# Kernel optimization log

Measured on AMD Instinct MI355X. Metric: run time of the kernel, lower is better.

Reference implementation:

```python
import jax, jax.numpy as jnp
import numpy as np

DIM, HEAD, FFN = 256, 4, 1024
NEG = -1e9


def layer_norm(x, g, b, eps=1e-5):
    mu = jnp.mean(x, axis=-1, keepdims=True)
    var = jnp.mean((x - mu) ** 2, axis=-1, keepdims=True)
    return (x - mu) / jnp.sqrt(var + eps) * g + b


def setup_inputs() -> dict:
    key = jax.random.key(0)
    ks = jax.random.split(key, 10)
    B, T, D = 8, 2048, DIM
    s = 1.0 / np.sqrt(D)
    x = jax.random.normal(ks[0], (B, T, D), dtype=jnp.float32)
    mask = jax.random.randint(ks[1], (B, T), 0, 2).astype(jnp.float32)
    Wqkv = jax.random.uniform(ks[2], (3 * D, D), jnp.float32, -s, s)
    bqkv = jnp.zeros((3 * D,), jnp.float32)
    Wo = jax.random.uniform(ks[3], (D, D), jnp.float32, -s, s)
    bo = jnp.zeros((D,), jnp.float32)
    W1 = jax.random.uniform(ks[4], (FFN, D), jnp.float32, -s, s)
    b1 = jnp.zeros((FFN,), jnp.float32)
    W2 = jax.random.uniform(ks[5], (D, FFN), jnp.float32, -1.0 / np.sqrt(FFN), 1.0 / np.sqrt(FFN))
    b2 = jnp.zeros((D,), jnp.float32)
    g1 = jnp.ones((D,), jnp.float32); be1 = jnp.zeros((D,), jnp.float32)
    g2 = jnp.ones((D,), jnp.float32); be2 = jnp.zeros((D,), jnp.float32)
    return dict(x=x, mask=mask, Wqkv=Wqkv, bqkv=bqkv, Wo=Wo, bo=bo,
                W1=W1, b1=b1, W2=W2, b2=b2, g1=g1, be1=be1, g2=g2, be2=be2)


def _forward(x, mask, Wqkv, bqkv, Wo, bo, W1, b1, W2, b2, g1, be1, g2, be2):
    B, T, D = x.shape
    H = HEAD
    hd = D // H
    # --- MultiheadAttention (explicit, non-flash path, need_weights=True) ---
    qkv = jnp.einsum('btd,ed->bte', x, Wqkv) + bqkv            # (B,T,3D)
    q, k, v = jnp.split(qkv, 3, axis=-1)
    q = q.reshape(B, T, H, hd).transpose(0, 2, 1, 3)           # (B,H,T,hd)
    k = k.reshape(B, T, H, hd).transpose(0, 2, 1, 3)
    v = v.reshape(B, T, H, hd).transpose(0, 2, 1, 3)
    scores = jnp.einsum('bhqd,bhkd->bhqk', q, k) / jnp.sqrt(jnp.float32(hd))
    scores = jnp.where(mask[:, None, None, :] > 0.5, NEG, scores)
    w = jax.nn.softmax(scores, axis=-1)                        # (B,H,T,T)
    attn = jnp.einsum('bhqk,bhkd->bhqd', w, v)                 # (B,H,T,hd)
    attn = attn.transpose(0, 2, 1, 3).reshape(B, T, D)
    attn_out = jnp.einsum('btd,ed->bte', attn, Wo) + bo        # (B,T,D)
    w_avg = jnp.mean(w, axis=1)                                # (B,T,T), averaged over heads
    # halting score: sum over query dim (dim=1), then masked softmax
    halting = jnp.sum(w_avg, axis=1)                           # (B,T)
    halting = jax.nn.softmax(halting + mask * (-1e10), axis=-1)
    # --- residual + LN + FFN + LN ---
    h = layer_norm(x + attn_out, g1, be1)
    ffn = jnp.einsum('btf,df->btd', jax.nn.relu(jnp.einsum('btd,fd->btf', h, W1) + b1), W2) + b2
    out = layer_norm(h + ffn, g2, be2)
    return out, halting


def reference(x, mask, Wqkv, bqkv, Wo, bo, W1, b1, W2, b2, g1, be1, g2, be2):
    return _forward(x, mask, Wqkv, bqkv, Wo, bo, W1, b1, W2, b2, g1, be1, g2, be2)
```

## Files before the change

kernel.cpp:

```cpp
#include <hip/hip_runtime.h>
#include <hip/hip_bf16.h>
#include <math.h>

namespace {

constexpr int B = 8, T = 2048, D = 256, H = 4, HD = 64, FF = 1024;
constexpr float QSCALE = 0.18033688f;

typedef __attribute__((ext_vector_type(8))) short short8;
typedef __attribute__((ext_vector_type(4))) short s16x4;
typedef __attribute__((ext_vector_type(4))) float f32x4;

__device__ __forceinline__ short f2bf(float f) {
    __hip_bfloat16 h = __float2bfloat16(f);
    return *reinterpret_cast<short*>(&h);
}
__device__ __forceinline__ float exp2a(float x) {
    float r; asm("v_exp_f32 %0, %1" : "=v"(r) : "v"(x)); return r;
}
__device__ __forceinline__ unsigned cvtpk(float lo, float hi) {
    unsigned r; asm("v_cvt_pk_bf16_f32 %0, %1, %2" : "=v"(r) : "v"(lo), "v"(hi)); return r;
}

__global__ __launch_bounds__(256) void k_cvt(
        const float* __restrict__ x,  const float* __restrict__ wq,
        const float* __restrict__ wo, const float* __restrict__ w1,
        const float* __restrict__ w2,
        short* __restrict__ x16,  short* __restrict__ wq16,
        short* __restrict__ wo16, short* __restrict__ w116,
        short* __restrict__ w216) {
    const int N0 = 524288, N1 = 24576, N2 = 8192, N3 = 32768, N4 = 32768;
    const int total = N0 + N1 + N2 + N3 + N4;
    for (int i = blockIdx.x*256 + threadIdx.x; i < total; i += gridDim.x*256) {
        const float* s; short* d; int j = i;
        if (j < N0) { s = x; d = x16; }
        else { j -= N0;
            if (j < N1) { s = wq; d = wq16; }
            else { j -= N1;
                if (j < N2) { s = wo; d = wo16; }
                else { j -= N2;
                    if (j < N3) { s = w1; d = w116; }
                    else { j -= N3; s = w2; d = w216; }
                }
            }
        }
        float4 a = ((const float4*)s)[j*2], b2 = ((const float4*)s)[j*2+1];
        short8 o;
        o[0]=f2bf(a.x);  o[1]=f2bf(a.y);  o[2]=f2bf(a.z);  o[3]=f2bf(a.w);
        o[4]=f2bf(b2.x); o[5]=f2bf(b2.y); o[6]=f2bf(b2.z); o[7]=f2bf(b2.w);
        ((short8*)d)[j] = o;
    }
}

template<int MODE>
__global__ __launch_bounds__(256) void k_gemm(
        const short* __restrict__ A, const short* __restrict__ W,
        const float* __restrict__ bias, const int K,
        short* __restrict__ oq, short* __restrict__ ok, short* __restrict__ ov,
        float* __restrict__ of, short* __restrict__ o16) {
    __shared__ short As[64][72];
    __shared__ short Ws[64][72];
    __shared__ float Cs[64][68];
    const int tid = threadIdx.x;
    const int w = tid >> 6, lane = tid & 63;
    const int qr = lane & 15, g = lane >> 4;
    const int wm = w >> 1, wn = w & 1;
    const int m0 = blockIdx.x * 64;
    const int n0 = blockIdx.y * 64;
    const int srow = tid >> 2, scol = (tid & 3) * 8;
    const short* Ag = A + (size_t)(m0 + srow) * K + scol;
    const short* Wg = W + (size_t)(n0 + srow) * K + scol;

    f32x4 acc[2][2];
    #pragma unroll
    for (int i = 0; i < 2; i++)
        #pragma unroll
        for (int j = 0; j < 2; j++) acc[i][j] = (f32x4){0.f, 0.f, 0.f, 0.f};

    for (int k0 = 0; k0 < K; k0 += 64) {
        __syncthreads();
        *(short8*)&As[srow][scol]      = *(const short8*)(Ag + k0);
        *(short8*)&As[srow][scol + 32] = *(const short8*)(Ag + k0 + 32);
        *(short8*)&Ws[srow][scol]      = *(const short8*)(Wg + k0);
        *(short8*)&Ws[srow][scol + 32] = *(const short8*)(Wg + k0 + 32);
        __syncthreads();
        #pragma unroll
        for (int kk = 0; kk < 2; kk++) {
            short8 a0 = *(const short8*)&As[wm*32 + qr][g*8 + kk*32];
            short8 a1 = *(const short8*)&As[wm*32 + 16 + qr][g*8 + kk*32];
            short8 b0 = *(const short8*)&Ws[wn*32 + qr][g*8 + kk*32];
            short8 b1 = *(const short8*)&Ws[wn*32 + 16 + qr][g*8 + kk*32];
            acc[0][0] = __builtin_amdgcn_mfma_f32_16x16x32_bf16(a0, b0, acc[0][0], 0, 0, 0);
            acc[0][1] = __builtin_amdgcn_mfma_f32_16x16x32_bf16(a0, b1, acc[0][1], 0, 0, 0);
            acc[1][0] = __builtin_amdgcn_mfma_f32_16x16x32_bf16(a1, b0, acc[1][0], 0, 0, 0);
            acc[1][1] = __builtin_amdgcn_mfma_f32_16x16x32_bf16(a1, b1, acc[1][1], 0, 0, 0);
        }
    }

    const int b = m0 >> 11;
    const int tl0 = m0 & (T - 1);

    if (MODE == 0 && blockIdx.y >= 8) {
        const int h = (int)blockIdx.y - 8;
        #pragma unroll
        for (int fm = 0; fm < 2; fm++) {
            const int tbase = tl0 + wm*32 + fm*16 + g*4;
            #pragma unroll
            for (int fn = 0; fn < 2; fn++) {
                const int d = wn*32 + fn*16 + qr;
                const float bv = bias[n0 + d];
                s16x4 pk;
                #pragma unroll
                for (int r = 0; r < 4; r++) pk[r] = f2bf(acc[fm][fn][r] + bv);
                *(s16x4*)&ov[((size_t)(b*H + h)*HD + d)*T + tbase] = pk;
            }
        }
        return;
    }

    #pragma unroll
    for (int fm = 0; fm < 2; fm++)
        #pragma unroll
        for (int fn = 0; fn < 2; fn++)
            #pragma unroll
            for (int r = 0; r < 4; r++)
                Cs[wm*32 + fm*16 + g*4 + r][wn*32 + fn*16 + qr] = acc[fm][fn][r];
    __syncthreads();
    const int row = tid >> 2, c0 = (tid & 3) * 16;
    float vals[16];
    #pragma unroll
    for (int j = 0; j < 16; j++) vals[j] = Cs[row][c0 + j] + bias[n0 + c0 + j];

    if (MODE == 0) {
        const int by = blockIdx.y;
        short* dst = (by < 4) ? oq : ok;
        const float qs = (by < 4) ? QSCALE : 1.0f;
        const int h = by & 3;
        short8 s0, s1;
        #pragma unroll
        for (int j = 0; j < 8; j++) { s0[j] = f2bf(vals[j]*qs); s1[j] = f2bf(vals[8+j]*qs); }
        short* p = dst + ((size_t)(b*H + h)*T + tl0 + row)*HD + c0;
        *(short8*)p = s0;
        *(short8*)(p + 8) = s1;
    } else if (MODE == 1 || MODE == 3) {
        float* p = of + (size_t)(m0 + row)*256 + n0 + c0;
        #pragma unroll
        for (int jj = 0; jj < 4; jj++) *(float4*)(p + jj*4) = *(float4*)&vals[jj*4];
    } else {
        short8 s0, s1;
        #pragma unroll
        for (int j = 0; j < 8; j++) {
            s0[j] = f2bf(fmaxf(vals[j], 0.f));
            s1[j] = f2bf(fmaxf(vals[8+j], 0.f));
        }
        short* p = o16 + (size_t)(m0 + row)*1024 + n0 + c0;
        *(short8*)p = s0;
        *(short8*)(p + 8) = s1;
    }
}

__global__ __launch_bounds__(256) void k_flashL(
        const short* __restrict__ qb, const short* __restrict__ kb,
        const float* __restrict__ mask, float* __restrict__ liout) {
    __shared__ short Ks[128][72];
    __shared__ float lbuf[4][4][16];
    const int tid = threadIdx.x;
    const int w = tid >> 6, lane = tid & 63;
    const int qr = lane & 15, g = lane >> 4;
    const int qt = blockIdx.x, h = blockIdx.y, b = blockIdx.z;
    const int bh = b*H + h;
    const int q0 = qt*64;

    short8 qf[4][2];
    {
        const short* qg = qb + ((size_t)bh * T + q0) * HD;
        #pragma unroll
        for (int qt4 = 0; qt4 < 4; qt4++) {
            qf[qt4][0] = *(const short8*)(qg + (qt4*16 + qr)*HD + g*8);
            qf[qt4][1] = *(const short8*)(qg + (qt4*16 + qr)*HD + 32 + g*8);
        }
    }
    const short* kg0 = kb + (size_t)bh * T * HD;
    const float* mg  = mask + (size_t)b * T;
    const int krow = lane >> 1, khalf = (lane & 1) * 32;

    float lrun[4] = {0.f, 0.f, 0.f, 0.f};

    for (int kt = 0; kt < 16; kt++) {
        const int kbase = kt*128 + w*32;
        {
            const short* ksrc = kg0 + (size_t)(kbase + krow)*HD + khalf;
            short* kdst = &Ks[w*32 + krow][khalf];
            #pragma unroll
            for (int c = 0; c < 4; c++)
                *(short8*)(kdst + c*8) = *(const short8*)(ksrc + c*8);
        }
        asm volatile("" ::: "memory");
        #pragma unroll
        for (int kt2 = 0; kt2 < 2; kt2++) {
            short8 kf0 = *(const short8*)&Ks[w*32 + kt2*16 + qr][g*8];
            short8 kf1 = *(const short8*)&Ks[w*32 + kt2*16 + qr][g*8 + 32];
            const int key0 = kbase + kt2*16;
            const float4 mv4 = *(const float4*)(mg + key0 + 4*g);
            const float b0 = (mv4.x > 0.5f) ? -1e9f : 0.f;
            const float b1 = (mv4.y > 0.5f) ? -1e9f : 0.f;
            const float b2v = (mv4.z > 0.5f) ? -1e9f : 0.f;
            const float b3 = (mv4.w > 0.5f) ? -1e9f : 0.f;
            #pragma unroll
            for (int qt4 = 0; qt4 < 4; qt4++) {
                f32x4 sa = (f32x4){b0, b1, b2v, b3};
                sa = __builtin_amdgcn_mfma_f32_16x16x32_bf16(kf0, qf[qt4][0], sa, 0, 0, 0);
                sa = __builtin_amdgcn_mfma_f32_16x16x32_bf16(kf1, qf[qt4][1], sa, 0, 0, 0);
                lrun[qt4] += (exp2a(sa[0]) + exp2a(sa[1])) + (exp2a(sa[2]) + exp2a(sa[3]));
            }
        }
        asm volatile("" ::: "memory");
    }
    #pragma unroll
    for (int qt4 = 0; qt4 < 4; qt4++) {
        lrun[qt4] += __shfl_xor(lrun[qt4], 16, 64);
        lrun[qt4] += __shfl_xor(lrun[qt4], 32, 64);
    }
    if (g == 0) {
        #pragma unroll
        for (int qt4 = 0; qt4 < 4; qt4++) lbuf[w][qt4][qr] = lrun[qt4];
    }
    __syncthreads();
    if (tid < 64) {
        const int qt4 = tid >> 4, qrr = tid & 15;
        const float l = lbuf[0][qt4][qrr] + lbuf[1][qt4][qrr]
                      + lbuf[2][qt4][qrr] + lbuf[3][qt4][qrr];
        liout[(size_t)bh*T + q0 + tid] = -__log2f(l);
    }
}

__global__ __launch_bounds__(256) void k_fattn(
        const short* __restrict__ qb, const short* __restrict__ kb,
        const short* __restrict__ vtb, const float* __restrict__ mask,
        const float* __restrict__ liout,
        short* __restrict__ attnb, float* __restrict__ part4) {
    __shared__ short Ks[128][72];
    __shared__ short Vt[64][136];
    __shared__ short Ps[4][64][40];
    const int tid = threadIdx.x;
    const int w = tid >> 6, lane = tid & 63;
    const int qr = lane & 15, g = lane >> 4;
    const int qt = blockIdx.x, h = blockIdx.y, b = blockIdx.z;
    const int bh = b*H + h;
    const int q0 = qt*64;

    short8 qf[4][2];
    float li[4];
    {
        const short* qg = qb + ((size_t)bh * T + q0) * HD;
        #pragma unroll
        for (int qt4 = 0; qt4 < 4; qt4++) {
            qf[qt4][0] = *(const short8*)(qg + (qt4*16 + qr)*HD + g*8);
            qf[qt4][1] = *(const short8*)(qg + (qt4*16 + qr)*HD + 32 + g*8);
            li[qt4] = liout[(size_t)bh*T + q0 + qt4*16 + qr];
        }
    }
    const short* kg0 = kb + (size_t)bh * T * HD;
    const short* vg0 = vtb + (size_t)bh * HD * T;
    const float* mg  = mask + (size_t)b * T;
    float* csrow = part4 + (size_t)(bh*32 + qt) * T;
    const int krow = lane >> 1, khalf = (lane & 1) * 32;

    f32x4 oa[4][4];
    #pragma unroll
    for (int nt = 0; nt < 4; nt++)
        #pragma unroll
        for (int qt4 = 0; qt4 < 4; qt4++) oa[nt][qt4] = (f32x4){0.f,0.f,0.f,0.f};

    short8 kreg[4], vreg[4];
    #pragma unroll
    for (int c = 0; c < 4; c++) {
        kreg[c] = *(const short8*)(kg0 + (size_t)(w*32 + krow)*HD + khalf + c*8);
        vreg[c] = *(const short8*)(vg0 + (size_t)lane*T + w*32 + c*8);
    }
    #pragma unroll
    for (int c = 0; c < 4; c++) {
        *(short8*)&Ks[w*32 + krow][khalf + c*8] = kreg[c];
        *(short8*)&Vt[lane][w*32 + c*8] = vreg[c];
    }
    asm volatile("" ::: "memory");

    for (int kt = 0; kt < 16; kt++) {
        if (kt < 15) {
            const int nb = (kt+1)*128 + w*32;
            #pragma unroll
            for (int c = 0; c < 4; c++) {
                kreg[c] = *(const short8*)(kg0 + (size_t)(nb + krow)*HD + khalf + c*8);
                vreg[c] = *(const short8*)(vg0 + (size_t)lane*T + nb + c*8);
            }
        }
        const int kbase = kt*128 + w*32;
        #pragma unroll
        for (int kt2 = 0; kt2 < 2; kt2++) {
            short8 kf0 = *(const short8*)&Ks[w*32 + kt2*16 + qr][g*8];
            short8 kf1 = *(const short8*)&Ks[w*32 + kt2*16 + qr][g*8 + 32];
            const int key0 = kbase + kt2*16;
            const float4 mv4 = *(const float4*)(mg + key0 + 4*g);
            const float mb[4] = { (mv4.x > 0.5f) ? -1e9f : 0.f,
                                  (mv4.y > 0.5f) ? -1e9f : 0.f,
                                  (mv4.z > 0.5f) ? -1e9f : 0.f,
                                  (mv4.w > 0.5f) ? -1e9f : 0.f };
            float p[4][4];
            #pragma unroll
            for (int qt4 = 0; qt4 < 4; qt4++) {
                f32x4 sa = (f32x4){mb[0] + li[qt4], mb[1] + li[qt4],
                                   mb[2] + li[qt4], mb[3] + li[qt4]};
                sa = __builtin_amdgcn_mfma_f32_16x16x32_bf16(kf0, qf[qt4][0], sa, 0, 0, 0);
                sa = __builtin_amdgcn_mfma_f32_16x16x32_bf16(kf1, qf[qt4][1], sa, 0, 0, 0);
                p[qt4][0] = exp2a(sa[0]); p[qt4][1] = exp2a(sa[1]);
                p[qt4][2] = exp2a(sa[2]); p[qt4][3] = exp2a(sa[3]);
            }
            float cs[4];
            #pragma unroll
            for (int r = 0; r < 4; r++) {
                cs[r] = (p[0][r] + p[1][r]) + (p[2][r] + p[3][r]);
                cs[r] += __shfl_xor(cs[r], 1, 64);
                cs[r] += __shfl_xor(cs[r], 2, 64);
                cs[r] += __shfl_xor(cs[r], 4, 64);
                cs[r] += __shfl_xor(cs[r], 8, 64);
            }
            if (qr == 0) {
                #pragma unroll
                for (int r = 0; r < 4; r++) csrow[key0 + 4*g + r] = cs[r];
            }
            #pragma unroll
            for (int qt4 = 0; qt4 < 4; qt4++) {
                union { unsigned u[2]; s16x4 s; } cv;
                cv.u[0] = cvtpk(p[qt4][0], p[qt4][1]);
                cv.u[1] = cvtpk(p[qt4][2], p[qt4][3]);
                *(s16x4*)&Ps[w][qt4*16 + qr][kt2*16 + 4*g] = cv.s;
            }
        }
        asm volatile("" ::: "memory");
        short8 pa[4];
        #pragma unroll
        for (int qt4 = 0; qt4 < 4; qt4++)
            pa[qt4] = *(const short8*)&Ps[w][qt4*16 + qr][g*8];
        #pragma unroll
        for (int nt = 0; nt < 4; nt++) {
            short8 vf = *(const short8*)&Vt[nt*16 + qr][w*32 + g*8];
            #pragma unroll
            for (int qt4 = 0; qt4 < 4; qt4++)
                oa[nt][qt4] = __builtin_amdgcn_mfma_f32_16x16x32_bf16(vf, pa[qt4], oa[nt][qt4], 0, 0, 0);
        }
        if (kt < 15) {
            asm volatile("" ::: "memory");
            #pragma unroll
            for (int c = 0; c < 4; c++) {
                *(short8*)&Ks[w*32 + krow][khalf + c*8] = kreg[c];
                *(short8*)&Vt[lane][w*32 + c*8] = vreg[c];
            }
            asm volatile("" ::: "memory");
        }
    }

    __syncthreads();
    float* Obuf = (float*)&Ks[0][0];
    const int qL = tid >> 2, dq = tid & 3;
    #pragma unroll
    for (int nt = 0; nt < 4; nt++) {
        #pragma unroll
        for (int qt4 = 0; qt4 < 4; qt4++)
            #pragma unroll
            for (int r = 0; r < 4; r++)
                Obuf[(w*16 + 4*g + r)*68 + qt4*16 + qr] = oa[nt][qt4][r];
        __syncthreads();
        s16x4 pk;
        #pragma unroll
        for (int rr = 0; rr < 4; rr++) {
            const int dr = dq*4 + rr;
            float v = Obuf[(0*16 + dr)*68 + qL] + Obuf[(1*16 + dr)*68 + qL]
                    + Obuf[(2*16 + dr)*68 + qL] + Obuf[(3*16 + dr)*68 + qL];
            pk[rr] = f2bf(v);
        }
        *(s16x4*)&attnb[((size_t)b*T + q0 + qL)*D + h*HD + nt*16 + dq*4] = pk;
        __syncthreads();
    }
}

__global__ __launch_bounds__(256) void k_red(
        const float* __restrict__ part, float* __restrict__ red) {
    __shared__ float s[128];
    const int b = blockIdx.y, kc = blockIdx.x;
    const int tid = threadIdx.x;
    const int c = tid & 127, half = tid >> 7;
    const int k = kc*128 + c;
    const float* pb = part + ((size_t)(b*128 + half*64))*T + k;
    float acc = 0.f;
    #pragma unroll 8
    for (int r = 0; r < 64; r++) acc += pb[(size_t)r*T];
    if (half) s[c] = acc;
    __syncthreads();
    if (!half) red[(size_t)b*T + k] = acc + s[c];
}

__global__ __launch_bounds__(256) void k_halt(
        const float* __restrict__ red, const float* __restrict__ mask,
        float* __restrict__ outh) {
    __shared__ float redm[4], reds[4];
    const int b = blockIdx.x, tid = threadIdx.x;
    const float* mg = mask + (size_t)b * T;
    float v[8];
    float M = -3e38f;
    #pragma unroll
    for (int i = 0; i < 8; i++) {
        v[i] = red[(size_t)b*T + tid + i*256]*0.25f + mg[tid + i*256]*(-1e10f);
        M = fmaxf(M, v[i]);
    }
    #pragma unroll
    for (int off = 1; off < 64; off <<= 1) M = fmaxf(M, __shfl_xor(M, off, 64));
    const int wv = tid >> 6, lane = tid & 63;
    if (lane == 0) redm[wv] = M;
    __syncthreads();
    M = fmaxf(fmaxf(redm[0], redm[1]), fmaxf(redm[2], redm[3]));
    float S = 0.f;
    #pragma unroll
    for (int i = 0; i < 8; i++) { v[i] = __expf(v[i] - M); S += v[i]; }
    #pragma unroll
    for (int off = 1; off < 64; off <<= 1) S += __shfl_xor(S, off, 64);
    if (lane == 0) reds[wv] = S;
    __syncthreads();
    const float invS = 1.f / (reds[0] + reds[1] + reds[2] + reds[3]);
    #pragma unroll
    for (int i = 0; i < 8; i++) outh[(size_t)b*T + tid + i*256] = v[i]*invS;
}

__global__ __launch_bounds__(256) void k_ln(
        const float* __restrict__ a, const float* __restrict__ bsrc,
        const float* __restrict__ g, const float* __restrict__ be,
        float* __restrict__ yf, short* __restrict__ y16) {
    __shared__ float s[16][D];
    const int tid = threadIdx.x;
    const size_t row0 = (size_t)blockIdx.x * 16;
    const float4* ag = (const float4*)(a + row0*D);
    const float4* bg = (const float4*)(bsrc + row0*D);
    #pragma unroll
    for (int i = 0; i < 4; i++) {
        float4 av = ag[tid + i*256], bv = bg[tid + i*256];
        float4 sv = {av.x+bv.x, av.y+bv.y, av.z+bv.z, av.w+bv.w};
        ((float4*)&s[0][0])[tid + i*256] = sv;
    }
    __syncthreads();
    const int wv = tid >> 6, lane = tid & 63;
    float gvv[4], bvv[4];
    #pragma unroll
    for (int s2 = 0; s2 < 4; s2++) { gvv[s2] = g[lane + 64*s2]; bvv[s2] = be[lane + 64*s2]; }
    #pragma unroll
    for (int rr = 0; rr < 4; rr++) {
        const int r = wv*4 + rr;
        float x0 = s[r][lane],     x1 = s[r][lane+64];
        float x2 = s[r][lane+128], x3 = s[r][lane+192];
        float sum = x0+x1+x2+x3;
        float ssq = x0*x0 + x1*x1 + x2*x2 + x3*x3;
        #pragma unroll
        for (int off = 1; off < 64; off <<= 1) {
            sum += __shfl_xor(sum, off, 64);
            ssq += __shfl_xor(ssq, off, 64);
        }
        const float mu = sum * (1.f/256.f);
        const float rs = rsqrtf(ssq*(1.f/256.f) - mu*mu + 1e-5f);
        float y0 = (x0 - mu)*rs*gvv[0] + bvv[0];
        float y1 = (x1 - mu)*rs*gvv[1] + bvv[1];
        float y2 = (x2 - mu)*rs*gvv[2] + bvv[2];
        float y3 = (x3 - mu)*rs*gvv[3] + bvv[3];
        float* yp = yf + (row0 + r)*D;
        yp[lane]     = y0;
        yp[lane+64]  = y1;
        yp[lane+128] = y2;
        yp[lane+192] = y3;
        if (y16) {
            short* hp = y16 + (row0 + r)*D;
            hp[lane]     = f2bf(y0);
            hp[lane+64]  = f2bf(y1);
            hp[lane+128] = f2bf(y2);
            hp[lane+192] = f2bf(y3);
        }
    }
}

}

extern "C" void kernel_launch(void* const* d_in, const int* in_sizes, int n_in,
                              void* d_out, int out_size, void* d_ws, size_t ws_size,
                              hipStream_t stream) {
    (void)in_sizes; (void)n_in; (void)out_size; (void)ws_size;
    const float* x    = (const float*)d_in[0];
    const float* mask = (const float*)d_in[1];
    const float* Wqkv = (const float*)d_in[2];
    const float* bqkv = (const float*)d_in[3];
    const float* Wo   = (const float*)d_in[4];
    const float* bo   = (const float*)d_in[5];
    const float* W1   = (const float*)d_in[6];
    const float* b1   = (const float*)d_in[7];
    const float* W2   = (const float*)d_in[8];
    const float* b2   = (const float*)d_in[9];
    const float* g1   = (const float*)d_in[10];
    const float* be1  = (const float*)d_in[11];
    const float* g2   = (const float*)d_in[12];
    const float* be2  = (const float*)d_in[13];

    float* out  = (float*)d_out;
    char*  wsb  = (char*)d_ws;
    const size_t MB = 1024*1024;

    short* qb16   = (short*)(wsb + 0*MB);
    short* kb16   = (short*)(wsb + 8*MB);
    short* vt16   = (short*)(wsb + 16*MB);
    short* x16    = (short*)(wsb + 24*MB);
    short* attn16 = (short*)(wsb + 24*MB);
    short* mid16  = (short*)(wsb + 0*MB);
    float* part4  = (float*)(wsb + 32*MB);
    float* redb   = (float*)(wsb + 40*MB);
    float* liout  = (float*)(wsb + 41*MB);
    short* wq16   = (short*)(wsb + 42*MB);
    short* wo16   = (short*)(wsb + 42*MB + 393216);
    short* w116   = (short*)(wsb + 42*MB + 524288);
    short* w216   = (short*)(wsb + 42*MB + 1048576);
    float* hb     = (float*)(wsb + 44*MB);
    short* h16    = (short*)(wsb + 60*MB);
    float* po     = (float*)(wsb + 68*MB);
    float* fo     = (float*)(wsb + 68*MB);
    float* outh   = out + (size_t)B*T*D;

    k_cvt    <<<dim3(1024),        256, 0, stream>>>(x, Wqkv, Wo, W1, W2,
                                                     x16, wq16, wo16, w116, w216);
    k_gemm<0><<<dim3(256, 12),     256, 0, stream>>>(x16, wq16, bqkv, 256,
                                                     qb16, kb16, vt16, nullptr, nullptr);
    k_flashL <<<dim3(32, H, B),    256, 0, stream>>>(qb16, kb16, mask, liout);
    k_fattn  <<<dim3(32, H, B),    256, 0, stream>>>(qb16, kb16, vt16, mask, liout,
                                                     attn16, part4);
    k_red    <<<dim3(16, B),       256, 0, stream>>>(part4, redb);
    k_halt   <<<dim3(B),           256, 0, stream>>>(redb, mask, outh);
    k_gemm<1><<<dim3(256, 4),      256, 0, stream>>>(attn16, wo16, bo, 256,
                                                     nullptr, nullptr, nullptr, po, nullptr);
    k_ln     <<<dim3(B*T/16),      256, 0, stream>>>(x, po, g1, be1, hb, h16);
    k_gemm<2><<<dim3(256, 16),     256, 0, stream>>>(h16, w116, b1, 256,
                                                     nullptr, nullptr, nullptr, nullptr, mid16);
    k_gemm<3><<<dim3(256, 4),      256, 0, stream>>>(mid16, w216, b2, 1024,
                                                     nullptr, nullptr, nullptr, fo, nullptr);
    k_ln     <<<dim3(B*T/16),      256, 0, stream>>>(hb, fo, g2, be2, out, nullptr);
}
```

Measured before the change: 230.6 us.

## Use 128x128 tiled GEMM with direct global-to-LDS loads for QKV and FFN1

```diff
diff --git a/kernel.cpp b/kernel.cpp
--- a/kernel.cpp
+++ b/kernel.cpp
@@ -20,6 +20,11 @@
 }
 __device__ __forceinline__ unsigned cvtpk(float lo, float hi) {
     unsigned r; asm("v_cvt_pk_bf16_f32 %0, %1, %2" : "=v"(r) : "v"(lo), "v"(hi)); return r;
+}
+__device__ __forceinline__ void gload16(const void* g, void* l) {
+    __builtin_amdgcn_global_load_lds(
+        (const __attribute__((address_space(1))) void*)g,
+        (__attribute__((address_space(3))) void*)l, 16, 0, 0);
 }
 
 __global__ __launch_bounds__(256) void k_cvt(
@@ -53,11 +58,146 @@
 }
 
 template<int MODE>
+__global__ __launch_bounds__(256) void k_gemm128(
+        const short* __restrict__ A, const short* __restrict__ W,
+        const float* __restrict__ bias, const int K,
+        short* __restrict__ oq, short* __restrict__ ok, short* __restrict__ ov,
+        short* __restrict__ o16) {
+    __shared__ char pool[34048];
+    short* Asl = (short*)pool;
+    short* Wsl = (short*)(pool + 16384);
+    float (*Cs)[133] = (float(*)[133])pool;
+
+    const int tid = threadIdx.x;
+    const int w = tid >> 6, lane = tid & 63;
+    const int qr = lane & 15, g = lane >> 4;
+    const int wm = w >> 1, wn = w & 1;
+    const int m0 = blockIdx.x * 128;
+    const int n0 = blockIdx.y * 128;
+    const int srow = lane >> 3;
+    const int scb  = (lane & 7) ^ srow;
+
+    f32x4 acc[4][4];
+    #pragma unroll
+    for (int i = 0; i < 4; i++)
+        #pragma unroll
+        for (int j = 0; j < 4; j++) acc[i][j] = (f32x4){0.f, 0.f, 0.f, 0.f};
+
+    for (int k0 = 0; k0 < K; k0 += 64) {
+        __syncthreads();
+        #pragma unroll
+        for (int i = 0; i < 4; i++) {
+            const int chunk = i*4 + w;
+            const int row = chunk*8 + srow;
+            gload16(A + (size_t)(m0 + row)*K + k0 + scb*8, Asl + chunk*512);
+            gload16(W + (size_t)(n0 + row)*K + k0 + scb*8, Wsl + chunk*512);
+        }
+        __syncthreads();
+        #pragma unroll
+        for (int kk = 0; kk < 2; kk++) {
+            const int swz = ((g + 4*kk) ^ (qr & 7)) * 8;
+            short8 af[4], bf[4];
+            #pragma unroll
+            for (int fm = 0; fm < 4; fm++)
+                af[fm] = *(const short8*)(Asl + (wm*64 + fm*16 + qr)*64 + swz);
+            #pragma unroll
+            for (int fn = 0; fn < 4; fn++)
+                bf[fn] = *(const short8*)(Wsl + (wn*64 + fn*16 + qr)*64 + swz);
+            #pragma unroll
+            for (int fm = 0; fm < 4; fm++)
+                #pragma unroll
+                for (int fn = 0; fn < 4; fn++)
+                    acc[fm][fn] = __builtin_amdgcn_mfma_f32_16x16x32_bf16(
+                        af[fm], bf[fn], acc[fm][fn], 0, 0, 0);
+        }
+    }
+
+    const int b = m0 >> 11;
+    const int tl0 = m0 & (T - 1);
+
+    if (MODE == 0 && blockIdx.y >= 4) {
+        #pragma unroll
+        for (int fm = 0; fm < 4; fm++) {
+            const int tl = tl0 + wm*64 + fm*16 + g*4;
+            #pragma unroll
+            for (int fn = 0; fn < 4; fn++) {
+                const int nv = (n0 - 512) + wn*64 + fn*16 + qr;
+                const int h = nv >> 6, d = nv & 63;
+                const float bv = bias[n0 + wn*64 + fn*16 + qr];
+                s16x4 pk;
+                #pragma unroll
+                for (int r = 0; r < 4; r++) pk[r] = f2bf(acc[fm][fn][r] + bv);
+                *(s16x4*)&ov[((size_t)(b*H + h)*HD + d)*T + tl] = pk;
+            }
+        }
+        return;
+    }
+
+    __syncthreads();
+    const int erow = tid & 63, c0 = (tid >> 6) * 32;
+    #pragma unroll
+    for (int hh = 0; hh < 2; hh++) {
+        if (wm == hh) {
+            #pragma unroll
+            for (int fm = 0; fm < 4; fm++)
+                #pragma unroll
+                for (int fn = 0; fn < 4; fn++)
+                    #pragma unroll
+                    for (int r = 0; r < 4; r++)
+                        Cs[fm*16 + g*4 + r][wn*64 + fn*16 + qr] = acc[fm][fn][r];
+        }
+        __syncthreads();
+        float vals[32];
+        #pragma unroll
+        for (int j = 0; j < 32; j++) vals[j] = Cs[erow][c0 + j] + bias[n0 + c0 + j];
+        const int tl = tl0 + hh*64 + erow;
+        if (MODE == 0) {
+            const int by = blockIdx.y;
+            short* dst = (by < 2) ? oq : ok;
+            const float qs = (by < 2) ? QSCALE : 1.0f;
+            const int h = (by & 1)*2 + (c0 >> 6);
+            const int d0 = c0 & 63;
+            short8 s0, s1;
+            #pragma unroll
+            for (int j = 0; j < 8; j++) {
+                s0[j] = f2bf(vals[j]*qs);
+                s1[j] = f2bf(vals[8+j]*qs);
+            }
+            short8 s2, s3;
+            #pragma unroll
+            for (int j = 0; j < 8; j++) {
+                s2[j] = f2bf(vals[16+j]*qs);
+                s3[j] = f2bf(vals[24+j]*qs);
+            }
+            short* p = dst + ((size_t)(b*H + h)*T + tl)*HD + d0;
+            *(short8*)p = s0;
+            *(short8*)(p + 8) = s1;
+            *(short8*)(p + 16) = s2;
+            *(short8*)(p + 24) = s3;
+        } else {
+            short8 s0, s1, s2, s3;
+            #pragma unroll
+            for (int j = 0; j < 8; j++) {
+                s0[j] = f2bf(fmaxf(vals[j],    0.f));
+                s1[j] = f2bf(fmaxf(vals[8+j],  0.f));
+                s2[j] = f2bf(fmaxf(vals[16+j], 0.f));
+                s3[j] = f2bf(fmaxf(vals[24+j], 0.f));
+            }
+            short* p = o16 + (size_t)(m0 + hh*64 + erow)*1024 + n0 + c0;
+            *(short8*)p = s0;
+            *(short8*)(p + 8) = s1;
+            *(short8*)(p + 16) = s2;
+            *(short8*)(p + 24) = s3;
+        }
+        if (hh == 0) __syncthreads();
+    }
+}
+
+template<int MODE>
 __global__ __launch_bounds__(256) void k_gemm(
         const short* __restrict__ A, const short* __restrict__ W,
         const float* __restrict__ bias, const int K,
-        short* __restrict__ oq, short* __restrict__ ok, short* __restrict__ ov,
-        float* __restrict__ of, short* __restrict__ o16) {
+        float* __restrict__ of) {
     __shared__ short As[64][72];
     __shared__ short Ws[64][72];
     __shared__ float Cs[64][68];
@@ -97,27 +237,6 @@
         }
     }
 
-    const int b = m0 >> 11;
-    const int tl0 = m0 & (T - 1);
-
-    if (MODE == 0 && blockIdx.y >= 8) {
-        const int h = (int)blockIdx.y - 8;
-        #pragma unroll
-        for (int fm = 0; fm < 2; fm++) {
-            const int tbase = tl0 + wm*32 + fm*16 + g*4;
-            #pragma unroll
-            for (int fn = 0; fn < 2; fn++) {
-                const int d = wn*32 + fn*16 + qr;
-                const float bv = bias[n0 + d];
-                s16x4 pk;
-                #pragma unroll
-                for (int r = 0; r < 4; r++) pk[r] = f2bf(acc[fm][fn][r] + bv);
-                *(s16x4*)&ov[((size_t)(b*H + h)*HD + d)*T + tbase] = pk;
-            }
-        }
-        return;
-    }
-
     #pragma unroll
     for (int fm = 0; fm < 2; fm++)
         #pragma unroll
@@ -130,33 +249,9 @@
     float vals[16];
     #pragma unroll
     for (int j = 0; j < 16; j++) vals[j] = Cs[row][c0 + j] + bias[n0 + c0 + j];
-
-    if (MODE == 0) {
-        const int by = blockIdx.y;
-        short* dst = (by < 4) ? oq : ok;
-        const float qs = (by < 4) ? QSCALE : 1.0f;
-        const int h = by & 3;
-        short8 s0, s1;
-        #pragma unroll
-        for (int j = 0; j < 8; j++) { s0[j] = f2bf(vals[j]*qs); s1[j] = f2bf(vals[8+j]*qs); }
-        short* p = dst + ((size_t)(b*H + h)*T + tl0 + row)*HD + c0;
-        *(short8*)p = s0;
-        *(short8*)(p + 8) = s1;
-    } else if (MODE == 1 || MODE == 3) {
-        float* p = of + (size_t)(m0 + row)*256 + n0 + c0;
-        #pragma unroll
-        for (int jj = 0; jj < 4; jj++) *(float4*)(p + jj*4) = *(float4*)&vals[jj*4];
-    } else {
-        short8 s0, s1;
-        #pragma unroll
-        for (int j = 0; j < 8; j++) {
-            s0[j] = f2bf(fmaxf(vals[j], 0.f));
-            s1[j] = f2bf(fmaxf(vals[8+j], 0.f));
-        }
-        short* p = o16 + (size_t)(m0 + row)*1024 + n0 + c0;
-        *(short8*)p = s0;
-        *(short8*)(p + 8) = s1;
-    }
+    float* p = of + (size_t)(m0 + row)*256 + n0 + c0;
+    #pragma unroll
+    for (int jj = 0; jj < 4; jj++) *(float4*)(p + jj*4) = *(float4*)&vals[jj*4];
 }
 
 __global__ __launch_bounds__(256) void k_flashL(
@@ -527,21 +622,19 @@
     float* fo     = (float*)(wsb + 68*MB);
     float* outh   = out + (size_t)B*T*D;
 
-    k_cvt    <<<dim3(1024),        256, 0, stream>>>(x, Wqkv, Wo, W1, W2,
-                                                     x16, wq16, wo16, w116, w216);
-    k_gemm<0><<<dim3(256, 12),     256, 0, stream>>>(x16, wq16, bqkv, 256,
-                                                     qb16, kb16, vt16, nullptr, nullptr);
-    k_flashL <<<dim3(32, H, B),    256, 0, stream>>>(qb16, kb16, mask, liout);
-    k_fattn  <<<dim3(32, H, B),    256, 0, stream>>>(qb16, kb16, vt16, mask, liout,
-                                                     attn16, part4);
-    k_red    <<<dim3(16, B),       256, 0, stream>>>(part4, redb);
-    k_halt   <<<dim3(B),           256, 0, stream>>>(redb, mask, outh);
-    k_gemm<1><<<dim3(256, 4),      256, 0, stream>>>(attn16, wo16, bo, 256,
-                                                     nullptr, nullptr, nullptr, po, nullptr);
-    k_ln     <<<dim3(B*T/16),      256, 0, stream>>>(x, po, g1, be1, hb, h16);
-    k_gemm<2><<<dim3(256, 16),     256, 0, stream>>>(h16, w116, b1, 256,
-                                                     nullptr, nullptr, nullptr, nullptr, mid16);
-    k_gemm<3><<<dim3(256, 4),      256, 0, stream>>>(mid16, w216, b2, 1024,
-                                                     nullptr, nullptr, nullptr, fo, nullptr);
-    k_ln     <<<dim3(B*T/16),      256, 0, stream>>>(hb, fo, g2, be2, out, nullptr);
-}
+    k_cvt      <<<dim3(1024),       256, 0, stream>>>(x, Wqkv, Wo, W1, W2,
+                                                      x16, wq16, wo16, w116, w216);
+    k_gemm128<0><<<dim3(128, 6),    256, 0, stream>>>(x16, wq16, bqkv, 256,
+                                                      qb16, kb16, vt16, nullptr);
+    k_flashL   <<<dim3(32, H, B),   256, 0, stream>>>(qb16, kb16, mask, liout);
+    k_fattn    <<<dim3(32, H, B),   256, 0, stream>>>(qb16, kb16, vt16, mask, liout,
+                                                      attn16, part4);
+    k_red      <<<dim3(16, B),      256, 0, stream>>>(part4, redb);
+    k_halt     <<<dim3(B),          256, 0, stream>>>(redb, mask, outh);
+    k_gemm<1>  <<<dim3(256, 4),     256, 0, stream>>>(attn16, wo16, bo, 256, po);
+    k_ln       <<<dim3(B*T/16),     256, 0, stream>>>(x, po, g1, be1, hb, h16);
+    k_gemm128<2><<<dim3(128, 8),    256, 0, stream>>>(h16, w116, b1, 256,
+                                                      nullptr, nullptr, nullptr, mid16);
+    k_gemm<3>  <<<dim3(256, 4),     256, 0, stream>>>(mid16, w216, b2, 1024, fo);
+    k_ln       <<<dim3(B*T/16),     256, 0, stream>>>(hb, fo, g2, be2, out, nullptr);
+}
```

Measured after the change: 231.5 us. Within noise of the previous version (+0.4%).
